# Kernel optimization log

Measured on AMD Instinct MI355X. Metric: run time of the kernel, lower is better.

Reference implementation:

```python
import jax, jax.numpy as jnp
import numpy as np

DIVERSITY = 1.0
DISPARITY_STEP = 2


def setup_inputs() -> dict:
    key = jax.random.key(0)
    k1, k2, k3 = jax.random.split(key, 3)
    B, D, H, W = 8, 64, 256, 512
    similarities = jax.random.normal(k1, (B, D, H, W), dtype=jnp.float32)
    max_disp = (D - 1) * DISPARITY_STEP  # 126
    gt = jax.random.uniform(k2, (B, H, W), dtype=jnp.float32) * max_disp
    unknown = jax.random.uniform(k3, (B, H, W)) < 0.05
    gt = jnp.where(unknown, jnp.inf, gt)
    return {"similarities": similarities, "ground_truth_disparities": gt}


def reference(similarities, ground_truth_disparities):
    # similarities: [B, D, H, W]; ground_truth_disparities: [B, H, W]
    D = similarities.shape[1]
    known = jnp.isfinite(ground_truth_disparities)           # [B, H, W]
    gt_safe = jnp.where(known, ground_truth_disparities, 0.0)
    log_P_pred = jax.nn.log_softmax(similarities, axis=1)    # [B, D, H, W]
    disparities = (jnp.arange(D, dtype=similarities.dtype)
                   * DISPARITY_STEP)[None, :, None, None]    # [1, D, 1, 1]
    # Unnormalized Laplace target centered at sub-pixel ground truth
    P_target = jnp.exp(-jnp.abs(gt_safe[:, None] - disparities) / DIVERSITY) \
               / (2.0 * DIVERSITY)                            # [B, D, H, W]
    sum_P_target = jnp.sum(P_target, axis=1)                  # [B, H, W]
    sum_Pt_logP = jnp.sum(P_target * log_P_pred, axis=1)      # [B, H, W]
    entropy = -sum_Pt_logP / sum_P_target                     # [B, H, W]
    # Mean over pixels with known ground truth (masked mean, jit-friendly)
    num_known = jnp.sum(known)
    return jnp.sum(jnp.where(known, entropy, 0.0)) / num_known
```

## Files before the change

### kernel.cpp

```cpp
#include <hip/hip_runtime.h>
#include <math.h>

constexpr int Bn = 8, Dn = 64, Hn = 256, Wn = 512;
constexpr int HW   = Hn * Wn;
constexpr int NPIX = Bn * HW;
constexpr int TPB  = 256;
constexpr int PPT  = 4;
constexpr int NBLK = NPIX / (TPB * PPT);

__global__ __launch_bounds__(TPB) void sce_main(const float* __restrict__ sim,
                                                const float* __restrict__ gt,
                                                float* __restrict__ acc) {
    const int tid = blockIdx.x * TPB + threadIdx.x;
    const int p0  = tid * PPT;
    const int b   = p0 / HW;
    const int rem = p0 - b * HW;
    const float4* simv = reinterpret_cast<const float4*>(sim + (size_t)b * Dn * HW + rem);
    const int dstride = HW / 4;

    const float4 g4 = *reinterpret_cast<const float4*>(gt + p0);
    float gg[4] = {g4.x, g4.y, g4.z, g4.w};

    float s[4]  = {0.f, 0.f, 0.f, 0.f};
    float S1[4] = {0.f, 0.f, 0.f, 0.f};
    float S2[4] = {0.f, 0.f, 0.f, 0.f};

#pragma unroll 8
    for (int d = 0; d < Dn; ++d) {
        float4 v4 = simv[(size_t)d * dstride];
        float v[4] = {v4.x, v4.y, v4.z, v4.w};
        const float dd = 2.0f * (float)d;
#pragma unroll
        for (int i = 0; i < 4; ++i) {
            s[i] += __expf(v[i]);
            float t = __expf(-fabsf(gg[i] - dd));
            S1[i] += t;
            S2[i] = fmaf(t, v[i], S2[i]);
        }
    }

    float lsum = 0.0f, lcnt = 0.0f;
#pragma unroll
    for (int i = 0; i < 4; ++i) {
        if (isfinite(gg[i])) {
            lsum += logf(s[i]) - S2[i] / S1[i];
            lcnt += 1.0f;
        }
    }

#pragma unroll
    for (int off = 32; off > 0; off >>= 1) {
        lsum += __shfl_down(lsum, off, 64);
        lcnt += __shfl_down(lcnt, off, 64);
    }

    __shared__ float ssum[TPB / 64], scnt[TPB / 64];
    const int lane = threadIdx.x & 63;
    const int wave = threadIdx.x >> 6;
    if (lane == 0) { ssum[wave] = lsum; scnt[wave] = lcnt; }
    __syncthreads();
    if (threadIdx.x == 0) {
        float bs = 0.f, bc = 0.f;
#pragma unroll
        for (int w = 0; w < TPB / 64; ++w) { bs += ssum[w]; bc += scnt[w]; }
        atomicAdd(&acc[0], bs);
        atomicAdd(&acc[1], bc);
    }
}

__global__ void sce_final(const float* __restrict__ acc, float* __restrict__ out) {
    out[0] = acc[0] / acc[1];
}

extern "C" void kernel_launch(void* const* d_in, const int* in_sizes, int n_in,
                              void* d_out, int out_size, void* d_ws, size_t ws_size,
                              hipStream_t stream) {
    const float* sim = (const float*)d_in[0];
    const float* gt  = (const float*)d_in[1];
    float* acc = (float*)d_ws;
    hipMemsetAsync(acc, 0, 2 * sizeof(float), stream);
    sce_main<<<NBLK, TPB, 0, stream>>>(sim, gt, acc);
    sce_final<<<1, 1, 0, stream>>>(acc, (float*)d_out);
}
```

Before: 373.0 us.

## Software-pipeline disparity loads, use nontemporal loads, fuse final division via ticket

```diff
diff --git a/kernel.cpp b/kernel.cpp
--- a/kernel.cpp
+++ b/kernel.cpp
@@ -7,43 +7,63 @@
 constexpr int TPB  = 256;
 constexpr int PPT  = 4;
 constexpr int NBLK = NPIX / (TPB * PPT);
+constexpr int UF   = 8;
+constexpr int NG   = Dn / UF;
+
+typedef float fx4 __attribute__((ext_vector_type(4)));
 
 __global__ __launch_bounds__(TPB) void sce_main(const float* __restrict__ sim,
                                                 const float* __restrict__ gt,
-                                                float* __restrict__ acc) {
+                                                float* __restrict__ accf,
+                                                unsigned* __restrict__ ticket,
+                                                float* __restrict__ out) {
     const int tid = blockIdx.x * TPB + threadIdx.x;
     const int p0  = tid * PPT;
     const int b   = p0 / HW;
     const int rem = p0 - b * HW;
-    const float4* simv = reinterpret_cast<const float4*>(sim + (size_t)b * Dn * HW + rem);
-    const int dstride = HW / 4;
+    const fx4* simv = reinterpret_cast<const fx4*>(sim + (size_t)b * Dn * HW + rem);
+    const int ds = HW / 4;
 
-    const float4 g4 = *reinterpret_cast<const float4*>(gt + p0);
+    const fx4 g4 = __builtin_nontemporal_load(reinterpret_cast<const fx4*>(gt + p0));
     float gg[4] = {g4.x, g4.y, g4.z, g4.w};
 
     float s[4]  = {0.f, 0.f, 0.f, 0.f};
     float S1[4] = {0.f, 0.f, 0.f, 0.f};
     float S2[4] = {0.f, 0.f, 0.f, 0.f};
 
-#pragma unroll 8
-    for (int d = 0; d < Dn; ++d) {
-        float4 v4 = simv[(size_t)d * dstride];
-        float v[4] = {v4.x, v4.y, v4.z, v4.w};
-        const float dd = 2.0f * (float)d;
+    fx4 cur[UF], nxt[UF];
 #pragma unroll
-        for (int i = 0; i < 4; ++i) {
-            s[i] += __expf(v[i]);
-            float t = __expf(-fabsf(gg[i] - dd));
-            S1[i] += t;
-            S2[i] = fmaf(t, v[i], S2[i]);
+    for (int i = 0; i < UF; ++i)
+        cur[i] = __builtin_nontemporal_load(&simv[(size_t)i * ds]);
+
+#pragma unroll
+    for (int g = 0; g < NG; ++g) {
+        if (g + 1 < NG) {
+#pragma unroll
+            for (int i = 0; i < UF; ++i)
+                nxt[i] = __builtin_nontemporal_load(&simv[(size_t)((g + 1) * UF + i) * ds]);
         }
+#pragma unroll
+        for (int i = 0; i < UF; ++i) {
+            const float dd = 2.0f * (float)(g * UF + i);
+            float v[4] = {cur[i].x, cur[i].y, cur[i].z, cur[i].w};
+#pragma unroll
+            for (int j = 0; j < 4; ++j) {
+                s[j] += __expf(v[j]);
+                float t = __expf(-fabsf(gg[j] - dd));
+                S1[j] += t;
+                S2[j] = fmaf(t, v[j], S2[j]);
+            }
+        }
+#pragma unroll
+        for (int i = 0; i < UF; ++i) cur[i] = nxt[i];
     }
 
     float lsum = 0.0f, lcnt = 0.0f;
 #pragma unroll
-    for (int i = 0; i < 4; ++i) {
-        if (isfinite(gg[i])) {
-            lsum += logf(s[i]) - S2[i] / S1[i];
+    for (int j = 0; j < 4; ++j) {
+        if (isfinite(gg[j])) {
+            lsum += __logf(s[j]) - S2[j] / S1[j];
             lcnt += 1.0f;
         }
     }
@@ -63,13 +83,17 @@
         float bs = 0.f, bc = 0.f;
 #pragma unroll
         for (int w = 0; w < TPB / 64; ++w) { bs += ssum[w]; bc += scnt[w]; }
-        atomicAdd(&acc[0], bs);
-        atomicAdd(&acc[1], bc);
+        atomicAdd(&accf[0], bs);
+        atomicAdd(&accf[1], bc);
+        __threadfence();
+        unsigned old = atomicAdd(ticket, 1u);
+        if (old == NBLK - 1) {
+            __threadfence();
+            float ts = atomicAdd(&accf[0], 0.0f);
+            float tc = atomicAdd(&accf[1], 0.0f);
+            out[0] = ts / tc;
+        }
     }
-}
-
-__global__ void sce_final(const float* __restrict__ acc, float* __restrict__ out) {
-    out[0] = acc[0] / acc[1];
 }
 
 extern "C" void kernel_launch(void* const* d_in, const int* in_sizes, int n_in,
@@ -77,8 +101,8 @@
                               hipStream_t stream) {
     const float* sim = (const float*)d_in[0];
     const float* gt  = (const float*)d_in[1];
-    float* acc = (float*)d_ws;
-    hipMemsetAsync(acc, 0, 2 * sizeof(float), stream);
-    sce_main<<<NBLK, TPB, 0, stream>>>(sim, gt, acc);
-    sce_final<<<1, 1, 0, stream>>>(acc, (float*)d_out);
+    float* accf = (float*)d_ws;
+    unsigned* ticket = (unsigned*)d_ws + 2;
+    hipMemsetAsync(d_ws, 0, 16, stream);
+    sce_main<<<NBLK, TPB, 0, stream>>>(sim, gt, accf, ticket, (float*)d_out);
 }
```

Result: no change. 374.9 us (+0.5%).
